# Kernel tuning notes

Hardware: AMD Instinct MI355X
Metric: run time of the kernel (lower is better)

## Reference

```python
import jax, jax.numpy as jnp
import numpy as np
from jax.scipy.linalg import expm

B, HW, SPP, C, H, W = 4, 16384, 3, 64, 128, 128
D_SH = 25
EPS = 1e-8

# color SH mask: higher degrees downweighted (from GaussianAdapter.__init__)
_SH_MASK = np.ones(D_SH, np.float32)
for _d in range(1, 5):
    _SH_MASK[_d * _d:(_d + 1) * (_d + 1)] = 0.1 * 0.25 ** _d

# --- e3nn-style SO(3) generators for wigner_D (precomputed in numpy) ---

def _su2_generators(j):
    m = np.arange(-j, j)
    raising = np.diag(-np.sqrt(j * (j + 1) - m * (m + 1)), k=-1).astype(np.complex128)
    m = np.arange(-j + 1, j + 1)
    lowering = np.diag(np.sqrt(j * (j + 1) - m * (m - 1)), k=1).astype(np.complex128)
    m = np.arange(-j, j + 1)
    return np.stack([0.5 * (raising + lowering), np.diag(1j * m), -0.5j * (raising - lowering)])

def _change_basis(l):
    q = np.zeros((2 * l + 1, 2 * l + 1), dtype=np.complex128)
    for m in range(-l, 0):
        q[l + m, l + abs(m)] = 1 / np.sqrt(2)
        q[l + m, l - abs(m)] = -1j / np.sqrt(2)
    q[l, l] = 1.0
    for m in range(1, l + 1):
        q[l + m, l + abs(m)] = (-1) ** m / np.sqrt(2)
        q[l + m, l - abs(m)] = 1j * (-1) ** m / np.sqrt(2)
    return (-1j) ** l * q

def _so3_generators(l):
    X = _su2_generators(l)
    Q = _change_basis(l)
    return np.real(np.conj(Q.T) @ X @ Q).astype(np.float32)

_SO3 = [_so3_generators(l) for l in range(5)]

# --- small math helpers ---

def _quat_to_mat(q):  # q: (..., 4) wxyz, pytorch3d convention
    r, i, j, k = q[..., 0], q[..., 1], q[..., 2], q[..., 3]
    s = 2.0 / jnp.sum(q * q, axis=-1)
    m = jnp.stack([
        1 - s * (j * j + k * k), s * (i * j - k * r), s * (i * k + j * r),
        s * (i * j + k * r), 1 - s * (i * i + k * k), s * (j * k - i * r),
        s * (i * k - j * r), s * (j * k + i * r), 1 - s * (i * i + j * j)], -1)
    return m.reshape(q.shape[:-1] + (3, 3))

def _rot_y(a):
    c, s = jnp.cos(a), jnp.sin(a)
    z, o = jnp.zeros_like(a), jnp.ones_like(a)
    return jnp.stack([jnp.stack([c, z, s], -1), jnp.stack([z, o, z], -1), jnp.stack([-s, z, c], -1)], -2)

def _rot_x(a):
    c, s = jnp.cos(a), jnp.sin(a)
    z, o = jnp.zeros_like(a), jnp.ones_like(a)
    return jnp.stack([jnp.stack([o, z, z], -1), jnp.stack([z, c, -s], -1), jnp.stack([z, s, c], -1)], -2)

def _matrix_to_angles(R):  # e3nn matrix_to_angles, YXY convention
    x = R[..., :, 1]  # R @ e_y
    x = x / jnp.linalg.norm(x, axis=-1, keepdims=True)
    beta = jnp.arccos(jnp.clip(x[..., 1], -1.0, 1.0))
    alpha = jnp.arctan2(x[..., 0], x[..., 2])
    A = _rot_y(alpha) @ _rot_x(beta)  # angles_to_matrix(alpha, beta, 0)
    Rp = jnp.swapaxes(A, -1, -2) @ R
    gamma = jnp.arctan2(Rp[..., 0, 2], Rp[..., 0, 0])
    return alpha, beta, gamma

def _wigner_D(l, alpha, beta, gamma):  # alpha/beta/gamma: [b]
    X = jnp.asarray(_SO3[l])
    ea = jax.vmap(expm)(alpha[:, None, None] * X[1])
    eb = jax.vmap(expm)(beta[:, None, None] * X[0])
    eg = jax.vmap(expm)(gamma[:, None, None] * X[1])
    return ea @ eb @ eg  # [b, 2l+1, 2l+1]

def _rotate_sh(sh, R):  # sh: [b,hw,spp,3,25], R: [b,3,3]
    alpha, beta, gamma = _matrix_to_angles(R)
    out = []
    for l in range(5):
        D = _wigner_D(l, alpha, -beta, gamma)
        out.append(jnp.einsum('bij,bhscj->bhsci', D, sh[..., l * l:(l + 1) * (l + 1)]))
    return jnp.concatenate(out, axis=-1)

def _forward(extrinsics, intrinsics, coordinates, depths, opacities, raw_gaussians, grd_feat, image_h, image_w):
    scales_raw = raw_gaussians[..., :3]
    rot_raw = raw_gaussians[..., 3:7]
    color_sh = raw_gaussians[..., 7:7 + 3 * D_SH]
    b, c, h, w = grd_feat.shape
    features = jnp.transpose(grd_feat.reshape(b, c, h * w), (0, 2, 1))[:, :, None, :]  # [b,hw,1,c]
    scales = 0.5 + (15.0 - 0.5) * jax.nn.sigmoid(scales_raw)
    pixel_size = jnp.array([1.0 / image_w, 1.0 / image_h], dtype=jnp.float32)
    K2inv = jnp.linalg.inv(intrinsics[..., :2, :2])
    multiplier = 0.1 * jnp.einsum('bij,j->bi', K2inv, pixel_size).sum(-1)  # [b]
    scales = scales * depths[..., None] * multiplier[:, None, None, None]
    rotations = rot_raw / (jnp.linalg.norm(rot_raw, axis=-1, keepdims=True) + EPS)
    color_sh = color_sh.reshape(color_sh.shape[:-1] + (3, D_SH)) * jnp.asarray(_SH_MASK)
    features = jnp.broadcast_to(features, opacities.shape + (c,))
    # covariance = R S S^T R^T
    Rq = _quat_to_mat(rotations)
    covariances = jnp.einsum('...ij,...j,...kj->...ik', Rq, scales * scales, Rq)
    # world rays
    Kinv = jnp.linalg.inv(intrinsics)
    coords_h = jnp.concatenate([coordinates, jnp.ones_like(coordinates[..., :1])], -1)
    dirs = jnp.einsum('bij,bhsj->bhsi', Kinv, coords_h)
    dirs = dirs / jnp.linalg.norm(dirs, axis=-1, keepdims=True)
    Rc2w = extrinsics[..., :3, :3]
    dirs = jnp.einsum('bij,bhsj->bhsi', Rc2w, dirs)
    origins = extrinsics[:, None, None, :3, 3]
    means = origins + dirs * depths[..., None]
    sh_rot = _rotate_sh(color_sh, Rc2w)
    rotations = jnp.broadcast_to(rotations, scales.shape[:-1] + (4,))
    return (means, covariances, sh_rot, opacities, features, scales, rotations)

def setup_inputs() -> dict:
    key = jax.random.key(0)
    ks = jax.random.split(key, 8)
    q = jax.random.normal(ks[0], (B, 4), jnp.float32)
    q = q / jnp.linalg.norm(q, axis=-1, keepdims=True)
    R = _quat_to_mat(q)
    t = jax.random.normal(ks[1], (B, 3), jnp.float32)
    extrinsics = jnp.tile(jnp.eye(4, dtype=jnp.float32), (B, 1, 1)).at[:, :3, :3].set(R).at[:, :3, 3].set(t)
    f = jax.random.uniform(ks[2], (B, 2), jnp.float32, 0.4, 0.6)
    intrinsics = (jnp.zeros((B, 3, 3), jnp.float32)
                  .at[:, 0, 0].set(f[:, 0]).at[:, 1, 1].set(f[:, 1])
                  .at[:, 0, 2].set(0.5).at[:, 1, 2].set(0.5).at[:, 2, 2].set(1.0))
    coordinates = jax.random.uniform(ks[3], (B, HW, SPP, 2), jnp.float32)
    depths = jax.random.uniform(ks[4], (B, HW, SPP), jnp.float32) * 50.0 + 0.5
    opacities = jax.random.uniform(ks[5], (B, HW, SPP), jnp.float32)
    raw_gaussians = jax.random.normal(ks[6], (B, HW, SPP, 3 + 4 + 3 * D_SH), jnp.float32)
    grd_feat = jax.random.normal(ks[7], (B, C, H, W), jnp.float32)
    return {"extrinsics": extrinsics, "intrinsics": intrinsics, "coordinates": coordinates,
            "depths": depths, "opacities": opacities, "raw_gaussians": raw_gaussians,
            "grd_feat": grd_feat, "image_h": H, "image_w": W}

def reference(extrinsics, intrinsics, coordinates, depths, opacities, raw_gaussians, grd_feat, image_h, image_w):
    return _forward(extrinsics, intrinsics, coordinates, depths, opacities, raw_gaussians, grd_feat, image_h, image_w)
```

## Files before the change

kernel.cpp:

```cpp
#include <hip/hip_runtime.h>
#include <math.h>

#define N_TOT   196608
#define HWSPP   49152
#define RGF     82
#define RGS     83
#define NGB     3072
#define NFB     1024

#define OFF_MEANS 0
#define OFF_COV   589824
#define OFF_SH    2359296
#define OFF_OP    17104896
#define OFF_FEAT  17301504
#define OFF_SCL   29884416
#define OFF_ROT   30474240

__device__ __constant__ int c_loff[5] = {0, 1, 10, 35, 84};

__device__ __forceinline__ float sigmoidf_(float x) { return 1.0f / (1.0f + expf(-x)); }

__global__ __launch_bounds__(64) void setup_kernel(
    const float* __restrict__ extr, const float* __restrict__ intr,
    const int* __restrict__ img_h, const int* __restrict__ img_w,
    float* __restrict__ ws)
{
  const int b = blockIdx.x / 5;
  const int l = blockIdx.x % 5;
  const int n = 2 * l + 1;
  const int nn = n * n;
  const int t = threadIdx.x;

  __shared__ double Qr[81], Qi[81], X0c[81];
  __shared__ double X0r[81], U[9];
  __shared__ double A_[81], P0[81], P1[81], E0[81], E1[81];

  const float* Ex = extr + b * 16;
  double R00 = Ex[0], R01 = Ex[1], R02 = Ex[2];
  double R11 = Ex[5];
  double R20 = Ex[8], R21 = Ex[9], R22 = Ex[10];
  double x0 = R01, x1 = R11, x2 = R21;
  double nr = sqrt(x0 * x0 + x1 * x1 + x2 * x2);
  x0 /= nr; x1 /= nr; x2 /= nr;
  double beta  = acos(fmin(1.0, fmax(-1.0, x1)));
  double alpha = atan2(x0, x2);
  double ca_ = cos(alpha), sa_ = sin(alpha);
  double gamma = atan2(ca_ * R02 - sa_ * R22, ca_ * R00 - sa_ * R20);

  if (l == 0 && t == 0) {
    const float* K = intr + b * 9;
    double k00=K[0],k01=K[1],k02=K[2],k10=K[3],k11=K[4],k12=K[5],k20=K[6],k21=K[7],k22=K[8];
    double det = k00*(k11*k22-k12*k21) - k01*(k10*k22-k12*k20) + k02*(k10*k21-k11*k20);
    double id = 1.0 / det;
    float* kv = ws + 660 + b * 9;
    kv[0] = (float)((k11*k22-k12*k21)*id);
    kv[1] = (float)((k02*k21-k01*k22)*id);
    kv[2] = (float)((k01*k12-k02*k11)*id);
    kv[3] = (float)((k12*k20-k10*k22)*id);
    kv[4] = (float)((k00*k22-k02*k20)*id);
    kv[5] = (float)((k02*k10-k00*k12)*id);
    kv[6] = (float)((k10*k21-k11*k20)*id);
    kv[7] = (float)((k01*k20-k00*k21)*id);
    kv[8] = (float)((k00*k11-k01*k10)*id);
    double d2 = k00 * k11 - k01 * k10;
    double ps0 = 1.0 / (double)img_w[0];
    double ps1 = 1.0 / (double)img_h[0];
    double sum = (k11 * ps0 - k01 * ps1 - k10 * ps0 + k00 * ps1) / d2;
    ws[696 + b] = (float)(0.1 * sum);
  }

  for (int e = t; e < 81; e += 64) { Qr[e] = 0.0; Qi[e] = 0.0; X0c[e] = 0.0; }
  __syncthreads();
  if (t == 0) {
    const double irt2 = 0.70710678118654752440;
    for (int m = -l; m < 0; ++m) {
      Qr[(l + m) * n + (l - m)] = irt2;
      Qi[(l + m) * n + (l + m)] = -irt2;
    }
    Qr[l * n + l] = 1.0;
    for (int m = 1; m <= l; ++m) {
      double sg = (m & 1) ? -1.0 : 1.0;
      Qr[(l + m) * n + (l + m)] = sg * irt2;
      Qi[(l + m) * n + (l - m)] = sg * irt2;
    }
    for (int i = 0; i < n - 1; ++i) {
      double mi = (double)(-l + i);
      double ci = sqrt((double)(l * (l + 1)) - mi * (mi + 1.0));
      X0c[i * n + (i + 1)] = 0.5 * ci;
      X0c[(i + 1) * n + i] = -0.5 * ci;
    }
  }
  __syncthreads();
  for (int e = t; e < nn; e += 64) {
    int i = e / n, j = e % n; double s = 0, s2 = 0;
    for (int k = 0; k < n; ++k) { s += X0c[i*n+k]*Qr[k*n+j]; s2 += X0c[i*n+k]*Qi[k*n+j]; }
    P0[e] = s; P1[e] = s2;
  }
  __syncthreads();
  for (int e = t; e < nn; e += 64) {
    int a = e / n, c = e % n; double s = 0;
    for (int r = 0; r < n; ++r) s += Qr[r*n+a]*P0[r*n+c] + Qi[r*n+a]*P1[r*n+c];
    X0r[e] = s;
  }
  if (t < n) {
    int i = t, j = 2 * l - i; double s1 = 0;
    for (int r = 0; r < n; ++r) {
      double mr = (double)(r - l);
      s1 += mr * (Qi[r*n+i]*Qr[r*n+j] - Qr[r*n+i]*Qi[r*n+j]);
    }
    U[i] = s1;
  }
  __syncthreads();

  const double ths = -beta / 64.0;
  for (int e = t; e < nn; e += 64) { A_[e] = ths * X0r[e]; P0[e] = A_[e]; }
  double Ereg[2];
  {
    int ii = 0;
    for (int e = t; e < nn; e += 64) { Ereg[ii++] = ((e/n)==(e%n) ? 1.0 : 0.0) + ths * X0r[e]; }
  }
  __syncthreads();
  double* Pc = P0; double* Pn = P1;
  for (int k = 2; k <= 12; ++k) {
    int ii = 0;
    for (int e = t; e < nn; e += 64) {
      int i = e / n, j = e % n; double s = 0;
      for (int kk = 0; kk < n; ++kk) s += Pc[i*n+kk] * A_[kk*n+j];
      s /= (double)k;
      Pn[e] = s; Ereg[ii++] += s;
    }
    __syncthreads();
    double* tmp = Pc; Pc = Pn; Pn = tmp;
  }
  {
    int ii = 0;
    for (int e = t; e < nn; e += 64) E0[e] = Ereg[ii++];
  }
  __syncthreads();
  double* Es = E0; double* Ed = E1;
  for (int q = 0; q < 6; ++q) {
    for (int e = t; e < nn; e += 64) {
      int i = e / n, j = e % n; double s = 0;
      for (int kk = 0; kk < n; ++kk) s += Es[i*n+kk] * Es[kk*n+j];
      Ed[e] = s;
    }
    __syncthreads();
    double* tmp = Es; Es = Ed; Ed = tmp;
  }

  for (int e = t; e < nn; e += 64) {
    int i = e / n, j = e % n;
    int i2 = 2 * l - i, j2 = 2 * l - j;
    double cai = cos(alpha * U[i]), sai = sin(alpha * U[i]);
    double cgj = cos(gamma * U[j]), sgj = sin(gamma * U[j]);
    double w1 = cgj * Es[i *n + j] - sgj * Es[i *n + j2];
    double w2 = cgj * Es[i2*n + j] - sgj * Es[i2*n + j2];
    ws[b * 165 + c_loff[l] + e] = (float)(cai * w1 + sai * w2);
  }
}

__global__ __launch_bounds__(256, 6) void main_kernel(
    const float* __restrict__ extr,
    const float* __restrict__ coords,
    const float* __restrict__ depths,
    const float* __restrict__ opac,
    const float* __restrict__ rg,
    const float* __restrict__ gf,
    const float* __restrict__ ws,
    float* __restrict__ out)
{
  __shared__ __align__(16) float smem[6784];
  const int t = threadIdx.x;
  const int bq = blockIdx.x >> 2;
  const int br = blockIdx.x & 3;

  if (br == 3) {
    float* tile = smem;
    const int b = bq >> 8;
    const int hw0 = (bq & 255) << 6;
    const int tx = t & 63, ty = t >> 6;
    const float* src = gf + (size_t)b * 64 * 16384 + hw0;
#pragma unroll
    for (int i = 0; i < 16; ++i) {
      int c = i * 4 + ty;
      tile[c * 65 + tx] = src[(size_t)c * 16384 + tx];
    }
    __syncthreads();
    float* dst = out + OFF_FEAT + ((size_t)(b * 16384 + hw0)) * 3 * 64;
    for (int r = ty; r < 192; r += 4) {
      int hw = r / 3;
      dst[(size_t)r * 64 + tx] = tile[tx * 65 + hw];
    }
    return;
  }

  const int gb = bq * 3 + br;
  float* sIn    = smem;
  float* sSmall = smem + 5312;
  float* sD     = smem + 6592;
  float* sKinv  = smem + 6757;
  float* sRc    = smem + 6766;
  float* sOrig  = smem + 6775;
  float* sMult  = smem + 6778;

  const int g0 = gb * 64;
  const int b  = g0 / HWSPP;

  float dpt = 0.f, opc = 0.f;
  float2 cxy = make_float2(0.f, 0.f);
  if (t < 64) {
    const int gidx = g0 + t;
    dpt = depths[gidx];
    opc = opac[gidx];
    cxy = ((const float2*)coords)[gidx];
  }

  if (t < 165) sD[t] = ws[b * 165 + t];
  else if (t < 174) sKinv[t - 165] = ws[660 + b * 9 + (t - 165)];
  else if (t < 183) { int k = t - 174; sRc[k] = extr[b * 16 + (k / 3) * 4 + (k % 3)]; }
  else if (t < 186) sOrig[t - 183] = extr[b * 16 + (t - 183) * 4 + 3];
  else if (t == 186) sMult[0] = ws[696 + b];

  {
    const float4* src4 = (const float4*)(rg + (size_t)g0 * RGF);
    for (int idx = t; idx < (64 * RGF) / 4; idx += 256) {
      float4 v = src4[idx];
      int base = idx * 4;
      int gg = base / RGF;
      int ff = base - gg * RGF;
      float vv[4] = {v.x, v.y, v.z, v.w};
#pragma unroll
      for (int e = 0; e < 4; ++e) {
        int g2 = gg, f2 = ff + e;
        if (f2 >= RGF) { g2 += 1; f2 -= RGF; }
        sIn[g2 * RGS + f2] = vv[e];
      }
    }
  }
  __syncthreads();

  float reg[25];
  int gg = 0, ch = 0;
  if (t < 64) {
    const float* q = &sIn[t * RGS];
#pragma unroll
    for (int j = 0; j < 7; ++j) reg[j] = q[j];
  } else {
    const int task = t - 64;
    gg = task & 63;
    ch = task >> 6;
    const float* shin = &sIn[gg * RGS + 7 + ch * 25];
#pragma unroll
    for (int j = 0; j < 25; ++j) reg[j] = shin[j];
  }
  __syncthreads();

  if (t < 64) {
    const float mlt = sMult[0];
    float sc0 = (0.5f + 14.5f * sigmoidf_(reg[0])) * dpt * mlt;
    float sc1 = (0.5f + 14.5f * sigmoidf_(reg[1])) * dpt * mlt;
    float sc2 = (0.5f + 14.5f * sigmoidf_(reg[2])) * dpt * mlt;
    float r0 = reg[3], r1 = reg[4], r2 = reg[5], r3 = reg[6];
    float nr = sqrtf(r0*r0 + r1*r1 + r2*r2 + r3*r3) + 1e-8f;
    float qr = r0/nr, qi = r1/nr, qj = r2/nr, qk = r3/nr;
    float s2 = 2.0f / (qr*qr + qi*qi + qj*qj + qk*qk);
    float R00 = 1.0f - s2*(qj*qj + qk*qk);
    float R01 = s2*(qi*qj - qk*qr);
    float R02 = s2*(qi*qk + qj*qr);
    float R10 = s2*(qi*qj + qk*qr);
    float R11 = 1.0f - s2*(qi*qi + qk*qk);
    float R12 = s2*(qj*qk - qi*qr);
    float R20 = s2*(qi*qk - qj*qr);
    float R21 = s2*(qj*qk + qi*qr);
    float R22 = 1.0f - s2*(qi*qi + qj*qj);
    float v0 = sc0*sc0, v1 = sc1*sc1, v2 = sc2*sc2;
    float C00 = R00*R00*v0 + R01*R01*v1 + R02*R02*v2;
    float C01 = R00*R10*v0 + R01*R11*v1 + R02*R12*v2;
    float C02 = R00*R20*v0 + R01*R21*v1 + R02*R22*v2;
    float C11 = R10*R10*v0 + R11*R11*v1 + R12*R12*v2;
    float C12 = R10*R20*v0 + R11*R21*v1 + R12*R22*v2;
    float C22 = R20*R20*v0 + R21*R21*v1 + R22*R22*v2;
    float dx = sKinv[0]*cxy.x + sKinv[1]*cxy.y + sKinv[2];
    float dy = sKinv[3]*cxy.x + sKinv[4]*cxy.y + sKinv[5];
    float dz = sKinv[6]*cxy.x + sKinv[7]*cxy.y + sKinv[8];
    float inr = 1.0f / sqrtf(dx*dx + dy*dy + dz*dz);
    dx *= inr; dy *= inr; dz *= inr;
    float wx = sRc[0]*dx + sRc[1]*dy + sRc[2]*dz;
    float wy = sRc[3]*dx + sRc[4]*dy + sRc[5]*dz;
    float wz = sRc[6]*dx + sRc[7]*dy + sRc[8]*dz;
    sSmall[t*3+0] = sOrig[0] + wx * dpt;
    sSmall[t*3+1] = sOrig[1] + wy * dpt;
    sSmall[t*3+2] = sOrig[2] + wz * dpt;
    float* cc = &sSmall[192 + t*9];
    cc[0]=C00; cc[1]=C01; cc[2]=C02; cc[3]=C01; cc[4]=C11; cc[5]=C12; cc[6]=C02; cc[7]=C12; cc[8]=C22;
    float* ss = &sSmall[768 + t*3]; ss[0]=sc0; ss[1]=sc1; ss[2]=sc2;
    float* rr = &sSmall[960 + t*4]; rr[0]=qr; rr[1]=qi; rr[2]=qj; rr[3]=qk;
    sSmall[1216 + t] = opc;
  } else {
    float* shout = &sIn[gg * 75 + ch * 25];
    shout[0] = sD[0] * reg[0];
#pragma unroll
    for (int i = 0; i < 3; ++i) {
      float a = sD[1+i*3]*reg[1] + sD[1+i*3+1]*reg[2] + sD[1+i*3+2]*reg[3];
      shout[1 + i] = (float)(0.1 * 0.25) * a;
    }
#pragma unroll
    for (int i = 0; i < 5; ++i) {
      float a = 0.f;
#pragma unroll
      for (int j = 0; j < 5; ++j) a += sD[10 + i*5 + j] * reg[4 + j];
      shout[4 + i] = (float)(0.1 * 0.0625) * a;
    }
#pragma unroll
    for (int i = 0; i < 7; ++i) {
      float a = 0.f;
#pragma unroll
      for (int j = 0; j < 7; ++j) a += sD[35 + i*7 + j] * reg[9 + j];
      shout[9 + i] = (float)(0.1 * 0.015625) * a;
    }
#pragma unroll
    for (int i = 0; i < 9; ++i) {
      float a = 0.f;
#pragma unroll
      for (int j = 0; j < 9; ++j) a += sD[84 + i*9 + j] * reg[16 + j];
      shout[16 + i] = (float)(0.1 * 0.00390625) * a;
    }
  }
  __syncthreads();

  {
    float4* osh = (float4*)(out + OFF_SH + (size_t)g0 * 75);
    const float4* s4 = (const float4*)sIn;
    for (int idx = t; idx < 1200; idx += 256) osh[idx] = s4[idx];
    float* om  = out + OFF_MEANS + (size_t)g0 * 3;
    float* oc  = out + OFF_COV   + (size_t)g0 * 9;
    float* os  = out + OFF_SCL   + (size_t)g0 * 3;
    float* orr = out + OFF_ROT   + (size_t)g0 * 4;
    float* oo  = out + OFF_OP    + (size_t)g0;
    if (t < 192) { om[t] = sSmall[t]; os[t] = sSmall[768 + t]; }
    for (int idx = t; idx < 576; idx += 256) oc[idx] = sSmall[192 + idx];
    orr[t] = sSmall[960 + t];
    if (t < 64) oo[t] = sSmall[1216 + t];
  }
}

extern "C" void kernel_launch(void* const* d_in, const int* in_sizes, int n_in,
                              void* d_out, int out_size, void* d_ws, size_t ws_size,
                              hipStream_t stream)
{
  const float* extr   = (const float*)d_in[0];
  const float* intr   = (const float*)d_in[1];
  const float* coords = (const float*)d_in[2];
  const float* depths = (const float*)d_in[3];
  const float* opac   = (const float*)d_in[4];
  const float* rg     = (const float*)d_in[5];
  const float* gf     = (const float*)d_in[6];
  const int*   ih     = (const int*)d_in[7];
  const int*   iw     = (const int*)d_in[8];
  float* out = (float*)d_out;
  float* ws  = (float*)d_ws;

  hipLaunchKernelGGL(setup_kernel, dim3(20), dim3(64), 0, stream, extr, intr, ih, iw, ws);
  hipLaunchKernelGGL(main_kernel, dim3(NGB + NFB), dim3(256), 0, stream,
                     extr, coords, depths, opac, rg, gf, ws, out);
}
```

Baseline: 240.1 us.

## Load raw gaussians via direct global-to-LDS DMA and vectorize feature and output copies

The raw gaussian staging loop, which did a float4 global load and then four scattered LDS stores into a padded 83-stride layout, is replaced with __builtin_amdgcn_global_load_lds. That copies 16 bytes per lane straight into an unpadded 82-stride LDS layout, plus a scalar tail for the last 512 bytes. The feature transpose branch now reads grd_feat with float4 loads, and the small per-gaussian outputs (means, cov, scale, rot, opacity) are written with float4 stores split across thread ranges. The aim is fewer VGPR round-trips and fewer global transactions. The cost is possible LDS bank conflicts from dropping the padding, and correctness depends on the global_load_lds wave-contiguous addressing matching the chosen layout.

```diff
diff --git a/kernel.cpp b/kernel.cpp
--- a/kernel.cpp
+++ b/kernel.cpp
@@ -4,7 +4,6 @@
 #define N_TOT   196608
 #define HWSPP   49152
 #define RGF     82
-#define RGS     83
 #define NGB     3072
 #define NFB     1024
 
@@ -19,6 +18,9 @@
 __device__ __constant__ int c_loff[5] = {0, 1, 10, 35, 84};
 
 __device__ __forceinline__ float sigmoidf_(float x) { return 1.0f / (1.0f + expf(-x)); }
+
+typedef __attribute__((address_space(3))) void lds_void;
+typedef __attribute__((address_space(1))) void gmem_void;
 
 __global__ __launch_bounds__(64) void setup_kernel(
     const float* __restrict__ extr, const float* __restrict__ intr,
@@ -169,7 +171,7 @@
     const float* __restrict__ ws,
     float* __restrict__ out)
 {
-  __shared__ __align__(16) float smem[6784];
+  __shared__ __align__(16) float smem[6720];
   const int t = threadIdx.x;
   const int bq = blockIdx.x >> 2;
   const int br = blockIdx.x & 3;
@@ -178,30 +180,33 @@
     float* tile = smem;
     const int b = bq >> 8;
     const int hw0 = (bq & 255) << 6;
+    const float4* src4 = (const float4*)(gf + (size_t)b * (64 * 16384) + hw0);
+#pragma unroll
+    for (int k = 0; k < 4; ++k) {
+      int flat = t + 256 * k;
+      int c = flat >> 4;
+      int j = flat & 15;
+      float4 v = src4[(size_t)c * 4096 + j];
+      float* tp = &tile[c * 65 + 4 * j];
+      tp[0] = v.x; tp[1] = v.y; tp[2] = v.z; tp[3] = v.w;
+    }
+    __syncthreads();
     const int tx = t & 63, ty = t >> 6;
-    const float* src = gf + (size_t)b * 64 * 16384 + hw0;
-#pragma unroll
-    for (int i = 0; i < 16; ++i) {
-      int c = i * 4 + ty;
-      tile[c * 65 + tx] = src[(size_t)c * 16384 + tx];
-    }
-    __syncthreads();
-    float* dst = out + OFF_FEAT + ((size_t)(b * 16384 + hw0)) * 3 * 64;
+    float* dst = out + OFF_FEAT + ((size_t)(b * 16384 + hw0)) * 192;
+    const float* trow = &tile[tx * 65];
     for (int r = ty; r < 192; r += 4) {
-      int hw = r / 3;
-      dst[(size_t)r * 64 + tx] = tile[tx * 65 + hw];
+      dst[(size_t)r * 64 + tx] = trow[r / 3];
     }
     return;
   }
 
   const int gb = bq * 3 + br;
-  float* sIn    = smem;
-  float* sSmall = smem + 5312;
-  float* sD     = smem + 6592;
-  float* sKinv  = smem + 6757;
-  float* sRc    = smem + 6766;
-  float* sOrig  = smem + 6775;
-  float* sMult  = smem + 6778;
+  float* sSmall = smem + 5248;
+  float* sD     = smem + 6528;
+  float* sKinv  = smem + 6693;
+  float* sRc    = smem + 6702;
+  float* sOrig  = smem + 6711;
+  float* sMult  = smem + 6714;
 
   const int g0 = gb * 64;
   const int b  = g0 / HWSPP;
@@ -222,34 +227,30 @@
   else if (t == 186) sMult[0] = ws[696 + b];
 
   {
-    const float4* src4 = (const float4*)(rg + (size_t)g0 * RGF);
-    for (int idx = t; idx < (64 * RGF) / 4; idx += 256) {
-      float4 v = src4[idx];
-      int base = idx * 4;
-      int gg = base / RGF;
-      int ff = base - gg * RGF;
-      float vv[4] = {v.x, v.y, v.z, v.w};
-#pragma unroll
-      for (int e = 0; e < 4; ++e) {
-        int g2 = gg, f2 = ff + e;
-        if (f2 >= RGF) { g2 += 1; f2 -= RGF; }
-        sIn[g2 * RGS + f2] = vv[e];
-      }
-    }
+    const char* gbase = (const char*)(rg + (size_t)g0 * RGF);
+    const int wbyte = (t & 192) << 4;
+#pragma unroll
+    for (int k = 0; k < 5; ++k) {
+      __builtin_amdgcn_global_load_lds(
+          (const gmem_void*)(gbase + ((size_t)(k * 256 + t) << 4)),
+          (lds_void*)((char*)smem + (k * 4096 + wbyte)),
+          16, 0, 0);
+    }
+    if (t < 32) ((float4*)smem)[1280 + t] = ((const float4*)gbase)[1280 + t];
   }
   __syncthreads();
 
   float reg[25];
   int gg = 0, ch = 0;
   if (t < 64) {
-    const float* q = &sIn[t * RGS];
+    const float* q = &smem[t * RGF];
 #pragma unroll
     for (int j = 0; j < 7; ++j) reg[j] = q[j];
   } else {
     const int task = t - 64;
     gg = task & 63;
     ch = task >> 6;
-    const float* shin = &sIn[gg * RGS + 7 + ch * 25];
+    const float* shin = &smem[gg * RGF + 7 + ch * 25];
 #pragma unroll
     for (int j = 0; j < 25; ++j) reg[j] = shin[j];
   }
@@ -297,7 +298,7 @@
     float* rr = &sSmall[960 + t*4]; rr[0]=qr; rr[1]=qi; rr[2]=qj; rr[3]=qk;
     sSmall[1216 + t] = opc;
   } else {
-    float* shout = &sIn[gg * 75 + ch * 25];
+    float* shout = &smem[gg * 75 + ch * 25];
     shout[0] = sD[0] * reg[0];
 #pragma unroll
     for (int i = 0; i < 3; ++i) {
@@ -329,18 +330,22 @@
   __syncthreads();
 
   {
+    const float4* s4 = (const float4*)smem;
     float4* osh = (float4*)(out + OFF_SH + (size_t)g0 * 75);
-    const float4* s4 = (const float4*)sIn;
     for (int idx = t; idx < 1200; idx += 256) osh[idx] = s4[idx];
-    float* om  = out + OFF_MEANS + (size_t)g0 * 3;
-    float* oc  = out + OFF_COV   + (size_t)g0 * 9;
-    float* os  = out + OFF_SCL   + (size_t)g0 * 3;
-    float* orr = out + OFF_ROT   + (size_t)g0 * 4;
-    float* oo  = out + OFF_OP    + (size_t)g0;
-    if (t < 192) { om[t] = sSmall[t]; os[t] = sSmall[768 + t]; }
-    for (int idx = t; idx < 576; idx += 256) oc[idx] = sSmall[192 + idx];
-    orr[t] = sSmall[960 + t];
-    if (t < 64) oo[t] = sSmall[1216 + t];
+
+    if (t < 144) {
+      ((float4*)(out + OFF_COV + (size_t)g0 * 9))[t] = ((const float4*)(sSmall + 192))[t];
+    } else if (t < 192) {
+      int i = t - 144;
+      ((float4*)(out + OFF_MEANS + (size_t)g0 * 3))[i] = ((const float4*)sSmall)[i];
+      ((float4*)(out + OFF_SCL   + (size_t)g0 * 3))[i] = ((const float4*)(sSmall + 768))[i];
+    } else {
+      int i = t - 192;
+      ((float4*)(out + OFF_ROT + (size_t)g0 * 4))[i] = ((const float4*)(sSmall + 960))[i];
+      if (i < 16)
+        ((float4*)(out + OFF_OP + (size_t)g0))[i] = ((const float4*)(sSmall + 1216))[i];
+    }
   }
 }
 
```

Measured after the change: 235.3 us. -2.0%, faster.
